# Kernel tuning notes

Measured on AMD Instinct MI355X. Metric: run time of the kernel, lower is better.

## Reference

```python
import jax, jax.numpy as jnp
import numpy as np

B, T, C = 2, 1024, 384
H, D = 4, 96            # heads, head_dim
BLK, NG = 16, 24        # HBS block size, num groups (NG*BLK == C)
SQ, PADM = 20, 400      # monarch grid dim, padded monarch dim
E, K, FF = 8, 2, 1536   # experts, top_k, expert hidden
EPS_LN = 1e-5


def _ln(x, g, b):
    m = jnp.mean(x, -1, keepdims=True)
    v = jnp.var(x, -1, keepdims=True)
    return (x - m) * jax.lax.rsqrt(v + EPS_LN) * g + b


def _hbs(x, pre_g, pre_b, blocks, wrow, wcol, alpha, bias):
    """HierarchicalBlockShuffleLayer: block mixing + flip + monarch, fp32."""
    orig = x.shape
    flat = _ln(x, pre_g, pre_b).astype(jnp.float32).reshape(-1, C)
    # block mixing: per-group 16x16 matmuls
    grouped = flat.reshape(-1, NG, BLK)
    y = jnp.einsum('ngb,gbc->ngc', grouped, blocks).reshape(-1, C)
    block_out = y[:, ::-1]  # torch.flip(dims=[-1])
    # monarch: pad to 400, view as 20x20 grid, left/right mix
    grid = jnp.pad(flat, ((0, 0), (0, PADM - C))).reshape(-1, SQ, SQ)
    z = jnp.einsum('nij,jk,lk->nil', grid, wcol, wrow)  # (x @ W_col) @ W_row.T
    mon = z.reshape(-1, PADM)[:, :C]
    out = block_out + alpha * mon + bias
    return out.reshape(orig)


def _rotary(t_len, d):
    inv = 1.0 / (10000.0 ** (jnp.arange(0, d, 2, dtype=jnp.float32) / d))
    fr = jnp.outer(jnp.arange(t_len, dtype=jnp.float32), inv)  # [T, d/2]
    emb = jnp.concatenate([fr, fr], -1)                        # [T, d]
    return jnp.cos(emb), jnp.sin(emb)


def _rotate_half(x):
    x1, x2 = x[..., : x.shape[-1] // 2], x[..., x.shape[-1] // 2:]
    return jnp.concatenate([-x2, x1], -1)


def _attention(xn, qkv_w, qkv_b, proj_pre_g, proj_pre_b, proj_blocks,
               proj_wrow, proj_wcol, proj_alpha, proj_bias,
               attn_norm_g, attn_norm_b, out_norm_g, out_norm_b, focus_gate):
    qkv = xn @ qkv_w + qkv_b  # [B,T,3C]
    q, k, v = jnp.split(qkv, 3, axis=-1)
    q = q.reshape(B, T, H, D).transpose(0, 2, 1, 3)  # bhtd
    k = k.reshape(B, T, H, D).transpose(0, 2, 1, 3)
    v = v.reshape(B, T, H, D).transpose(0, 2, 1, 3)
    cos, sin = _rotary(T, D)
    cos, sin = cos[None, None], sin[None, None]
    q = q * cos + _rotate_half(q) * sin
    k = k * cos + _rotate_half(k) * sin
    scale = 1.0 / jnp.sqrt(jnp.float32(D))
    # ---- linear attention branch (fp32, cumsum recurrence) ----
    Qp = jax.nn.elu(q * scale) + 1.0
    Kp = jax.nn.elu(k * scale) + 1.0
    KV = Kp[..., :, None] * v[..., None, :]          # bhtde
    KVc = jnp.cumsum(KV, axis=2)
    Kc = jnp.cumsum(Kp, axis=2)
    num = jnp.einsum('bhtd,bhtde->bhte', Qp, KVc)
    den = jnp.einsum('bhtd,bhtd->bht', Qp, Kc)[..., None]
    y_lin = num / (den + 1e-4)
    y_lin = _ln(y_lin, attn_norm_g, attn_norm_b)     # LN over head_dim
    # ---- sharp causal SDPA branch ----
    scores = jnp.einsum('bhtd,bhsd->bhts', q, k) * scale
    mask = jnp.tril(jnp.ones((T, T), dtype=bool))
    scores = jnp.where(mask, scores, -jnp.inf)
    y_sharp = jnp.einsum('bhts,bhsd->bhtd', jax.nn.softmax(scores, -1), v)
    # ---- gated combine ----
    a = jax.nn.sigmoid(focus_gate)
    y = a * y_sharp + (1.0 - a) * y_lin
    y = y.transpose(0, 2, 1, 3).reshape(B, T, C)
    y = _ln(y, out_norm_g, out_norm_b)
    return _hbs(y, proj_pre_g, proj_pre_b, proj_blocks, proj_wrow, proj_wcol,
                proj_alpha, proj_bias)


def _moe(xn, gate_w, w1, b1, w2, b2):
    xf = xn.reshape(-1, C)  # [N,C]
    logits = jnp.clip(xf @ gate_w, -20.0, 20.0)
    w, idx = jax.lax.top_k(logits, K)
    w = jax.nn.softmax(w, -1)
    # dense per-token expert weights [N,E] (same math as sparse dispatch, eval mode)
    wfull = jnp.sum(jax.nn.one_hot(idx, E, dtype=xf.dtype) * w[..., None], axis=1)
    h = jax.nn.gelu(jnp.einsum('nc,ech->neh', xf, w1) + b1, approximate=False)
    o = jnp.einsum('neh,ehc->nec', h, w2) + b2
    out = jnp.einsum('nec,ne->nc', o, wfull)
    return out.reshape(B, T, C)


def setup_inputs() -> dict:
    key = jax.random.key(0)
    ks = jax.random.split(key, 10)
    s = 0.02
    return {
        'x': jax.random.normal(ks[0], (B, T, C), jnp.float32),
        'ln1_g': jnp.ones((C,), jnp.float32), 'ln1_b': jnp.zeros((C,), jnp.float32),
        'ln2_g': jnp.ones((C,), jnp.float32), 'ln2_b': jnp.zeros((C,), jnp.float32),
        'qkv_w': jax.random.normal(ks[1], (C, 3 * C), jnp.float32) * s,
        'qkv_b': jnp.zeros((3 * C,), jnp.float32),
        'proj_pre_g': jnp.ones((C,), jnp.float32), 'proj_pre_b': jnp.zeros((C,), jnp.float32),
        'proj_blocks': jax.random.normal(ks[2], (NG, BLK, BLK), jnp.float32) * 0.125,
        'proj_wrow': jax.random.normal(ks[3], (SQ, SQ), jnp.float32) * 0.05,
        'proj_wcol': jax.random.normal(ks[4], (SQ, SQ), jnp.float32) * 0.05,
        'proj_alpha': jnp.zeros((), jnp.float32),
        'proj_bias': jnp.zeros((C,), jnp.float32),
        'attn_norm_g': jnp.ones((D,), jnp.float32), 'attn_norm_b': jnp.zeros((D,), jnp.float32),
        'out_norm_g': jnp.ones((C,), jnp.float32), 'out_norm_b': jnp.zeros((C,), jnp.float32),
        'focus_gate': jnp.zeros((), jnp.float32),
        'gate_w': jax.random.normal(ks[5], (C, E), jnp.float32) * s,
        'moe_w1': jax.random.normal(ks[6], (E, C, FF), jnp.float32) * s,
        'moe_b1': jnp.zeros((E, FF), jnp.float32),
        'moe_w2': jax.random.normal(ks[7], (E, FF, C), jnp.float32) * s,
        'moe_b2': jnp.zeros((E, C), jnp.float32),
    }


def reference(x, ln1_g, ln1_b, ln2_g, ln2_b, qkv_w, qkv_b,
              proj_pre_g, proj_pre_b, proj_blocks, proj_wrow, proj_wcol,
              proj_alpha, proj_bias, attn_norm_g, attn_norm_b,
              out_norm_g, out_norm_b, focus_gate, gate_w,
              moe_w1, moe_b1, moe_w2, moe_b2):
    h = x + _attention(_ln(x, ln1_g, ln1_b), qkv_w, qkv_b, proj_pre_g, proj_pre_b,
                       proj_blocks, proj_wrow, proj_wcol, proj_alpha, proj_bias,
                       attn_norm_g, attn_norm_b, out_norm_g, out_norm_b, focus_gate)
    out = h + _moe(_ln(h, ln2_g, ln2_b), gate_w, moe_w1, moe_b1, moe_w2, moe_b2)
    return out
```

## Files before the change

### kernel.cpp

```cpp
#include <hip/hip_runtime.h>
#include <math.h>

#define BB 2
#define TT 1024
#define CC 384
#define HH 4
#define DD 96
#define EE 8
#define FFD 1536
#define NROW (BB*TT)
#define QKVN (3*CC)
#define NSLOT (NROW*2)

typedef float f32x4 __attribute__((ext_vector_type(4)));
typedef short bf16x8 __attribute__((ext_vector_type(8)));

__device__ __forceinline__ float wredSum64(float v) {
#pragma unroll
  for (int o = 32; o > 0; o >>= 1) v += __shfl_xor(v, o, 64);
  return v;
}
__device__ __forceinline__ float rsum16(float v) {
#pragma unroll
  for (int o = 8; o > 0; o >>= 1) v += __shfl_xor(v, o, 16);
  return v;
}
__device__ __forceinline__ float rmax16(float v) {
#pragma unroll
  for (int o = 8; o > 0; o >>= 1) v = fmaxf(v, __shfl_xor(v, o, 16));
  return v;
}
__device__ __forceinline__ float dot4f(const float4 a, const float4 b) {
  return a.x*b.x + a.y*b.y + a.z*b.z + a.w*b.w;
}
__device__ __forceinline__ float blockRed128(float v, float* red) {
  v = wredSum64(v);
  const int w = threadIdx.x >> 6;
  if ((threadIdx.x & 63) == 0) red[w] = v;
  __syncthreads();
  float r = red[0] + red[1];
  __syncthreads();
  return r;
}
__device__ __forceinline__ float elup1(float x) {
  return x > 0.f ? x + 1.f : expf(x);
}
__device__ __forceinline__ unsigned short f2bf(float f) {
  unsigned int u = __float_as_uint(f);
  u = (u + 0x7FFFu + ((u >> 16) & 1u)) >> 16;
  return (unsigned short)u;
}

__global__ void zero_counts_kernel(int* counts) {
  if (threadIdx.x < EE) counts[threadIdx.x] = 0;
}

__global__ __launch_bounds__(256) void transconv_kernel(
    const float* __restrict__ src, unsigned short* __restrict__ dst,
    int K, int N) {
  src += (size_t)blockIdx.z * K * N;
  dst += (size_t)blockIdx.z * K * N;
  const int k0 = blockIdx.y * 32, n0 = blockIdx.x * 32;
  __shared__ float tile[32][33];
  const int t = threadIdx.x;
  const int ki = t >> 3, nj = (t & 7) * 4;
  const float4 v = *(const float4*)&src[(size_t)(k0 + ki) * N + n0 + nj];
  tile[ki][nj] = v.x; tile[ki][nj + 1] = v.y;
  tile[ki][nj + 2] = v.z; tile[ki][nj + 3] = v.w;
  __syncthreads();
  const int ni = t >> 3, kj = (t & 7) * 4;
  ushort4 o;
  o.x = f2bf(tile[kj][ni]);     o.y = f2bf(tile[kj + 1][ni]);
  o.z = f2bf(tile[kj + 2][ni]); o.w = f2bf(tile[kj + 3][ni]);
  *(ushort4*)&dst[(size_t)(n0 + ni) * K + k0 + kj] = o;
}

__global__ __launch_bounds__(64) void ln_row_kernel(
    const float* __restrict__ xin, const float* __restrict__ g,
    const float* __restrict__ b, float* __restrict__ xout) {
  const int row = blockIdx.x;
  const int lane = threadIdx.x;
  const size_t base = (size_t)row * CC;
  float v[6];
#pragma unroll
  for (int p = 0; p < 6; ++p) v[p] = xin[base + lane + 64 * p];
  float s = v[0] + v[1] + v[2] + v[3] + v[4] + v[5];
  s = wredSum64(s);
  const float mu = s * (1.f / CC);
  float sq = 0.f;
#pragma unroll
  for (int p = 0; p < 6; ++p) { float d = v[p] - mu; sq += d * d; }
  sq = wredSum64(sq);
  const float rinv = rsqrtf(sq * (1.f / CC) + 1e-5f);
#pragma unroll
  for (int p = 0; p < 6; ++p) {
    const int c = lane + 64 * p;
    xout[base + c] = (v[p] - mu) * rinv * g[c] + b[c];
  }
}

__global__ __launch_bounds__(256) void gemm_qkv_kernel(
    const float* __restrict__ A, const float* __restrict__ Bw,
    const float* __restrict__ bias, float* __restrict__ Cout) {
  const int N = QKVN, K = CC;
  const int n0 = blockIdx.x * 64, m0 = blockIdx.y * 64;
  __shared__ float As[16][68];
  __shared__ float Bs[16][64];
  const int tid = threadIdx.x, tx = tid & 15, ty = tid >> 4;
  const int am = tid >> 2, akq = (tid & 3) * 4;
  const int bkk = tid >> 4, bn4 = (tid & 15) * 4;
  float acc[4][4] = {};
  for (int k0 = 0; k0 < K; k0 += 16) {
    const float4 av4 = *(const float4*)&A[(size_t)(m0 + am) * K + k0 + akq];
    As[akq + 0][am] = av4.x; As[akq + 1][am] = av4.y;
    As[akq + 2][am] = av4.z; As[akq + 3][am] = av4.w;
    *(float4*)&Bs[bkk][bn4] =
        *(const float4*)&Bw[(size_t)(k0 + bkk) * N + n0 + bn4];
    __syncthreads();
#pragma unroll
    for (int kk = 0; kk < 16; ++kk) {
      const float4 av = *(const float4*)&As[kk][ty * 4];
      const float4 bv = *(const float4*)&Bs[kk][tx * 4];
      const float aa[4] = {av.x, av.y, av.z, av.w};
      const float bb4[4] = {bv.x, bv.y, bv.z, bv.w};
#pragma unroll
      for (int i = 0; i < 4; ++i)
#pragma unroll
        for (int jj = 0; jj < 4; ++jj) acc[i][jj] += aa[i] * bb4[jj];
    }
    __syncthreads();
  }
#pragma unroll
  for (int i = 0; i < 4; ++i) {
    const int r = m0 + ty * 4 + i;
#pragma unroll
    for (int jj = 0; jj < 4; ++jj) {
      const int c = n0 + tx * 4 + jj;
      Cout[(size_t)r * N + c] = acc[i][jj] + bias[c];
    }
  }
}

__global__ __launch_bounds__(256) void rope_kernel(
    const float* __restrict__ qkv, float* __restrict__ qr, float* __restrict__ kr,
    float* __restrict__ qp, float* __restrict__ kp) {
  const int gid = blockIdx.x * 256 + threadIdx.x;
  const int i = gid % 48;
  const int t = (gid / 48) % TT;
  const int h = (gid / (48 * TT)) % HH;
  const int b = gid / (48 * TT * HH);
  const float inv = 1.0f / powf(10000.0f, (float)i * (1.0f / 48.0f));
  const float ang = (float)t * inv;
  float sn, cs;
  sincosf(ang, &sn, &cs);
  const float* row = qkv + ((size_t)(b * TT + t)) * QKVN + h * DD;
  const float q1 = row[i], q2 = row[i + 48];
  const float k1 = row[CC + i], k2 = row[CC + i + 48];
  const float qo1 = q1 * cs - q2 * sn, qo2 = q2 * cs + q1 * sn;
  const float ko1 = k1 * cs - k2 * sn, ko2 = k2 * cs + k1 * sn;
  const size_t ob = ((size_t)((b * HH + h) * TT + t)) * DD;
  qr[ob + i] = qo1; qr[ob + i + 48] = qo2;
  kr[ob + i] = ko1; kr[ob + i + 48] = ko2;
  const float scale = 0.10206207261596577f;
  qp[ob + i] = elup1(qo1 * scale); qp[ob + i + 48] = elup1(qo2 * scale);
  kp[ob + i] = elup1(ko1 * scale); kp[ob + i + 48] = elup1(ko2 * scale);
}

__global__ __launch_bounds__(128, 3) void attn_kernel(
    const float* __restrict__ qr, const float* __restrict__ kr,
    const float* __restrict__ qp, const float* __restrict__ kp,
    const float* __restrict__ qkv, const float* __restrict__ ang,
    const float* __restrict__ anb, const float* __restrict__ fgp,
    float* __restrict__ y_attn) {
  __shared__ float Qt[16][100];
  __shared__ float Qpt[16][100];
  __shared__ float Kt[32][100];
  __shared__ float Kpt[32][100];
  __shared__ float Vt[32][100];
  __shared__ float Ps[16][34];
  __shared__ float Pl[16][34];
  const int idx = blockIdx.x;
  const int qt = 63 - (idx >> 3);
  const int bh = idx & 7, b = bh >> 2, h = bh & 3;
  const int tid = threadIdx.x;
  const int j = tid & 15;
  const int r = tid >> 4;
  const float a = 1.f / (1.f + expf(-fgp[0]));
  const int t0 = qt << 4;
  const size_t qbase = ((size_t)bh * TT + t0) * DD;
#pragma unroll
  for (int p = 0; p < 3; ++p) {
    const int i4 = tid + 128 * p, s = i4 / 24, d4 = (i4 % 24) * 4;
    *(float4*)&Qt[s][d4]  = *(const float4*)&qr[qbase + i4 * 4];
    *(float4*)&Qpt[s][d4] = *(const float4*)&qp[qbase + i4 * 4];
  }
  float accS[2][6] = {}, accN[2][6] = {};
  float mrow[2] = {-1e30f, -1e30f}, lrow[2] = {0.f, 0.f}, den[2] = {0.f, 0.f};
  const int nc = (qt >> 1) + 1;
  __syncthreads();
  for (int c = 0; c < nc; ++c) {
    const int s0 = c << 5;
    const float* vb = qkv + ((size_t)(b * TT + s0)) * QKVN + 2 * CC + h * DD;
    const size_t kb = ((size_t)bh * TT + s0) * DD;
#pragma unroll
    for (int p = 0; p < 6; ++p) {
      const int i4 = tid + 128 * p, s = i4 / 24, d4 = (i4 % 24) * 4;
      *(float4*)&Kt[s][d4]  = *(const float4*)&kr[kb + i4 * 4];
      *(float4*)&Kpt[s][d4] = *(const float4*)&kp[kb + i4 * 4];
      *(float4*)&Vt[s][d4]  = *(const float4*)&vb[(size_t)s * QKVN + d4];
    }
    __syncthreads();
    float ds00 = 0, ds01 = 0, ds10 = 0, ds11 = 0;
    float dl00 = 0, dl01 = 0, dl10 = 0, dl11 = 0;
#pragma unroll
    for (int dd = 0; dd < 96; dd += 4) {
      const float4 qa = *(const float4*)&Qt[r][dd];
      const float4 qb = *(const float4*)&Qt[r + 8][dd];
      const float4 ka = *(const float4*)&Kt[j][dd];
      const float4 k2 = *(const float4*)&Kt[j + 16][dd];
      ds00 += dot4f(qa, ka); ds01 += dot4f(qa, k2);
      ds10 += dot4f(qb, ka); ds11 += dot4f(qb, k2);
      const float4 pa = *(const float4*)&Qpt[r][dd];
      const float4 pb = *(const float4*)&Qpt[r + 8][dd];
      const float4 fa = *(const float4*)&Kpt[j][dd];
      const float4 f2 = *(const float4*)&Kpt[j + 16][dd];
      dl00 += dot4f(pa, fa); dl01 += dot4f(pa, f2);
      dl10 += dot4f(pb, fa); dl11 += dot4f(pb, f2);
    }
    const float scale = 0.10206207261596577f;
    float sc00 = ds00 * scale, sc01 = ds01 * scale;
    float sc10 = ds10 * scale, sc11 = ds11 * scale;
    if (c == nc - 1) {
      if (s0 + j > t0 + r)          { sc00 = -1e30f; dl00 = 0.f; }
      if (s0 + j + 16 > t0 + r)     { sc01 = -1e30f; dl01 = 0.f; }
      if (s0 + j > t0 + r + 8)      { sc10 = -1e30f; dl10 = 0.f; }
      if (s0 + j + 16 > t0 + r + 8) { sc11 = -1e30f; dl11 = 0.f; }
    }
    {
      const float cm = rmax16(fmaxf(sc00, sc01));
      const float mn = fmaxf(mrow[0], cm);
      const float sf = expf(mrow[0] - mn);
      const float p0 = expf(sc00 - mn), p1 = expf(sc01 - mn);
      lrow[0] = lrow[0] * sf + rsum16(p0 + p1);
      mrow[0] = mn;
      den[0] += rsum16(dl00 + dl01);
#pragma unroll
      for (int u = 0; u < 6; ++u) accS[0][u] *= sf;
      Ps[r][j] = p0; Ps[r][j + 16] = p1;
      Pl[r][j] = dl00; Pl[r][j + 16] = dl01;
    }
    {
      const float cm = rmax16(fmaxf(sc10, sc11));
      const float mn = fmaxf(mrow[1], cm);
      const float sf = expf(mrow[1] - mn);
      const float p0 = expf(sc10 - mn), p1 = expf(sc11 - mn);
      lrow[1] = lrow[1] * sf + rsum16(p0 + p1);
      mrow[1] = mn;
      den[1] += rsum16(dl10 + dl11);
#pragma unroll
      for (int u = 0; u < 6; ++u) accS[1][u] *= sf;
      Ps[r + 8][j] = p0; Ps[r + 8][j + 16] = p1;
      Pl[r + 8][j] = dl10; Pl[r + 8][j + 16] = dl11;
    }
    __syncthreads();
    const int c0 = j * 6;
#pragma unroll
    for (int s = 0; s < 32; s += 2) {
      const float2 pA = *(const float2*)&Ps[r][s];
      const float2 pB = *(const float2*)&Ps[r + 8][s];
      const float2 lA = *(const float2*)&Pl[r][s];
      const float2 lB = *(const float2*)&Pl[r + 8][s];
      const float* v0p = &Vt[s][c0];
      const float* v1p = v0p + 100;
      float va[6], vb2[6];
      *(float2*)&va[0] = *(const float2*)(v0p);
      *(float2*)&va[2] = *(const float2*)(v0p + 2);
      *(float2*)&va[4] = *(const float2*)(v0p + 4);
      *(float2*)&vb2[0] = *(const float2*)(v1p);
      *(float2*)&vb2[2] = *(const float2*)(v1p + 2);
      *(float2*)&vb2[4] = *(const float2*)(v1p + 4);
#pragma unroll
      for (int u = 0; u < 6; ++u) {
        accS[0][u] += pA.x * va[u] + pA.y * vb2[u];
        accS[1][u] += pB.x * va[u] + pB.y * vb2[u];
        accN[0][u] += lA.x * va[u] + lA.y * vb2[u];
        accN[1][u] += lB.x * va[u] + lB.y * vb2[u];
      }
    }
    __syncthreads();
  }
#pragma unroll
  for (int ri = 0; ri < 2; ++ri) {
    const int t = t0 + r + 8 * ri;
    const float invl = 1.0f / lrow[ri];
    const float dinv = 1.0f / (den[ri] + 1e-4f);
    float yl[6];
    float s1 = 0.f;
#pragma unroll
    for (int u = 0; u < 6; ++u) { yl[u] = accN[ri][u] * dinv; s1 += yl[u]; }
    s1 = rsum16(s1);
    const float mu = s1 * (1.f / DD);
    float s2 = 0.f;
#pragma unroll
    for (int u = 0; u < 6; ++u) { const float d = yl[u] - mu; s2 += d * d; }
    s2 = rsum16(s2);
    const float rr = rsqrtf(s2 * (1.f / DD) + 1e-5f);
    const size_t ob = ((size_t)(b * TT + t)) * CC + h * DD + j * 6;
#pragma unroll
    for (int u = 0; u < 6; ++u) {
      const float ylin = (yl[u] - mu) * rr * ang[j * 6 + u] + anb[j * 6 + u];
      const float ys = accS[ri][u] * invl;
      y_attn[ob + u] = a * ys + (1.f - a) * ylin;
    }
  }
}

__global__ __launch_bounds__(128) void hbs_kernel(
    const float* __restrict__ y_attn, const float* __restrict__ x,
    const float* __restrict__ outg, const float* __restrict__ outb,
    const float* __restrict__ preg, const float* __restrict__ preb,
    const float* __restrict__ blocks, const float* __restrict__ wrow,
    const float* __restrict__ wcol, const float* __restrict__ alphap,
    const float* __restrict__ biasv, const float* __restrict__ ln2g,
    const float* __restrict__ ln2b, const float* __restrict__ gatew,
    float* __restrict__ hout, unsigned short* __restrict__ xn2,
    int* __restrict__ tok_idx, float* __restrict__ tok_w, int* __restrict__ counts) {
  __shared__ float flatS[CC];
  __shared__ float ybuf[CC];
  __shared__ float xbuf[CC];
  __shared__ float tmp[400];
  __shared__ float red[2];
  __shared__ float logit[EE];
  const int row = blockIdx.x, tid = threadIdx.x;
  const size_t base = (size_t)row * CC;
  float v[3];
#pragma unroll
  for (int p = 0; p < 3; ++p) v[p] = y_attn[base + tid + 128 * p];
  float s = blockRed128(v[0] + v[1] + v[2], red);
  float mu = s * (1.f / CC);
  float sq = 0.f;
#pragma unroll
  for (int p = 0; p < 3; ++p) { const float d = v[p] - mu; sq += d * d; }
  sq = blockRed128(sq, red);
  float rin = rsqrtf(sq * (1.f / CC) + 1e-5f);
  float w[3];
#pragma unroll
  for (int p = 0; p < 3; ++p) {
    const int c = tid + 128 * p;
    w[p] = (v[p] - mu) * rin * outg[c] + outb[c];
  }
  s = blockRed128(w[0] + w[1] + w[2], red);
  mu = s * (1.f / CC);
  sq = 0.f;
#pragma unroll
  for (int p = 0; p < 3; ++p) { const float d = w[p] - mu; sq += d * d; }
  sq = blockRed128(sq, red);
  rin = rsqrtf(sq * (1.f / CC) + 1e-5f);
#pragma unroll
  for (int p = 0; p < 3; ++p) {
    const int c = tid + 128 * p;
    flatS[c] = (w[p] - mu) * rin * preg[c] + preb[c];
  }
  __syncthreads();
#pragma unroll
  for (int p = 0; p < 3; ++p) {
    const int o = tid + 128 * p;
    const int g = o >> 4, cc = o & 15;
    const float* bp = blocks + g * 256 + cc;
    const float* fp = flatS + g * 16;
    float acc = 0.f;
#pragma unroll
    for (int bb = 0; bb < 16; ++bb) acc += fp[bb] * bp[bb * 16];
    ybuf[o] = acc;
  }
#pragma unroll
  for (int p = 0; p < 4; ++p) {
    const int o = tid + 128 * p;
    if (o < 400) {
      const int i = o / 20, k = o - i * 20;
      float acc = 0.f;
#pragma unroll
      for (int jj = 0; jj < 20; ++jj) {
        const int src = i * 20 + jj;
        const float gv = (src < CC) ? flatS[src] : 0.f;
        acc += gv * wcol[jj * 20 + k];
      }
      tmp[o] = acc;
    }
  }
  __syncthreads();
  const float alpha = alphap[0];
  float hr[3];
#pragma unroll
  for (int p = 0; p < 3; ++p) {
    const int o = tid + 128 * p;
    const int i = o / 20, ll = o - i * 20;
    float mon = 0.f;
#pragma unroll
    for (int k = 0; k < 20; ++k) mon += tmp[i * 20 + k] * wrow[ll * 20 + k];
    const float hb = ybuf[383 - o] + alpha * mon + biasv[o];
    const float hv = x[base + o] + hb;
    hout[base + o] = hv;
    hr[p] = hv;
  }
  s = blockRed128(hr[0] + hr[1] + hr[2], red);
  mu = s * (1.f / CC);
  sq = 0.f;
#pragma unroll
  for (int p = 0; p < 3; ++p) { const float d = hr[p] - mu; sq += d * d; }
  sq = blockRed128(sq, red);
  rin = rsqrtf(sq * (1.f / CC) + 1e-5f);
#pragma unroll
  for (int p = 0; p < 3; ++p) {
    const int c = tid + 128 * p;
    const float xv = (hr[p] - mu) * rin * ln2g[c] + ln2b[c];
    xn2[base + c] = f2bf(xv);
    xbuf[c] = xv;
  }
  __syncthreads();
  const int e = tid >> 4, jj = tid & 15;
  float part = 0.f;
  for (int c = jj; c < CC; c += 16) part += xbuf[c] * gatew[c * EE + e];
  part = rsum16(part);
  if (jj == 0) logit[e] = fminf(20.f, fmaxf(-20.f, part));
  __syncthreads();
  if (tid == 0) {
    float lg[EE];
#pragma unroll
    for (int ee = 0; ee < EE; ++ee) lg[ee] = logit[ee];
    int i0 = 0; float v0 = lg[0];
#pragma unroll
    for (int ee = 1; ee < EE; ++ee) if (lg[ee] > v0) { v0 = lg[ee]; i0 = ee; }
    int i1 = -1; float v1 = -1e30f;
#pragma unroll
    for (int ee = 0; ee < EE; ++ee)
      if (ee != i0 && lg[ee] > v1) { v1 = lg[ee]; i1 = ee; }
    const float e1 = expf(v1 - v0);
    const float w0 = 1.f / (1.f + e1), w1 = e1 / (1.f + e1);
    tok_idx[2 * row] = i0; tok_idx[2 * row + 1] = i1;
    tok_w[2 * row] = w0; tok_w[2 * row + 1] = w1;
    atomicAdd(&counts[i0], 1);
    atomicAdd(&counts[i1], 1);
  }
}

__global__ void r_offsets_kernel(const int* __restrict__ counts, int* offsets, int* cursor) {
  if (threadIdx.x == 0) {
    int acc = 0;
    for (int e = 0; e < EE; ++e) { offsets[e] = acc; cursor[e] = acc; acc += counts[e]; }
  }
}
__global__ __launch_bounds__(256) void r_scatter_kernel(
    const int* __restrict__ tok_idx, const float* __restrict__ tok_w,
    int* cursor, int* __restrict__ perm, float* __restrict__ slotw,
    int* __restrict__ dest) {
  const int n = blockIdx.x * 256 + threadIdx.x;
  if (n >= NROW) return;
#pragma unroll
  for (int k = 0; k < 2; ++k) {
    const int e = tok_idx[2 * n + k];
    const int pos = atomicAdd(&cursor[e], 1);
    perm[pos] = n;
    slotw[pos] = tok_w[2 * n + k];
    dest[pos] = 2 * n + k;
  }
}


__global__ __launch_bounds__(256) void gemm_moe1_kernel(
    const unsigned short* __restrict__ xn2b, const unsigned short* __restrict__ w1t,
    const float* __restrict__ b1, const int* __restrict__ perm,
    const int* __restrict__ offsets, const int* __restrict__ counts,
    unsigned short* __restrict__ hbuf) {
  const int e = blockIdx.z;
  const int cnt = counts[e];
  const int m0 = blockIdx.y * 64;
  if (m0 >= cnt) return;
  const int n0 = blockIdx.x * 64;
  const int off = offsets[e];
  __shared__ __align__(16) short As[64][40];
  __shared__ __align__(16) short Bs[64][40];
  const int t = threadIdx.x;
  const int srow = t >> 2, sko = (t & 3) * 8;
  const int w = t >> 6, lane = t & 63, lm = lane & 15, kg8 = (lane >> 4) * 8;
  const int wr = (w >> 1) * 32, wc = (w & 1) * 32;
  const int sm = m0 + srow;
  const int grow = perm[off + (sm < cnt ? sm : cnt - 1)];
  const unsigned short* aro = xn2b + (size_t)grow * CC;
  const unsigned short* bro = w1t + ((size_t)e * FFD + n0 + srow) * CC;
  f32x4 acc[2][2] = {};
  for (int k0 = 0; k0 < CC; k0 += 32) {
    *(float4*)&As[srow][sko] = *(const float4*)(aro + k0 + sko);
    *(float4*)&Bs[srow][sko] = *(const float4*)(bro + k0 + sko);
    __syncthreads();
    const bf16x8 a0 = *(const bf16x8*)&As[wr + lm][kg8];
    const bf16x8 a1 = *(const bf16x8*)&As[wr + lm + 16][kg8];
    const bf16x8 b0 = *(const bf16x8*)&Bs[wc + lm][kg8];
    const bf16x8 b1v = *(const bf16x8*)&Bs[wc + lm + 16][kg8];
    acc[0][0] = __builtin_amdgcn_mfma_f32_16x16x32_bf16(a0, b0, acc[0][0], 0, 0, 0);
    acc[0][1] = __builtin_amdgcn_mfma_f32_16x16x32_bf16(a0, b1v, acc[0][1], 0, 0, 0);
    acc[1][0] = __builtin_amdgcn_mfma_f32_16x16x32_bf16(a1, b0, acc[1][0], 0, 0, 0);
    acc[1][1] = __builtin_amdgcn_mfma_f32_16x16x32_bf16(a1, b1v, acc[1][1], 0, 0, 0);
    __syncthreads();
  }
#pragma unroll
  for (int mi = 0; mi < 2; ++mi)
#pragma unroll
    for (int r = 0; r < 4; ++r) {
      const int m = m0 + wr + mi * 16 + (lane >> 4) * 4 + r;
      if (m < cnt) {
#pragma unroll
        for (int ni = 0; ni < 2; ++ni) {
          const int c = n0 + wc + ni * 16 + lm;
          const float tv = acc[mi][ni][r] + b1[e * FFD + c];
          const float gel = 0.5f * tv * (1.0f + erff(tv * 0.70710678118654752f));
          hbuf[(size_t)(off + m) * FFD + c] = f2bf(gel);
        }
      }
    }
}

__global__ __launch_bounds__(256) void gemm_moe2_kernel(
    const unsigned short* __restrict__ hbuf, const unsigned short* __restrict__ w2t,
    const float* __restrict__ b2, const int* __restrict__ offsets,
    const int* __restrict__ counts, const int* __restrict__ dest,
    const float* __restrict__ slotw, float* __restrict__ so) {
  const int e = blockIdx.z;
  const int cnt = counts[e];
  const int m0 = blockIdx.y * 64;
  if (m0 >= cnt) return;
  const int n0 = blockIdx.x * 64;
  const int off = offsets[e];
  __shared__ __align__(16) short As[64][40];
  __shared__ __align__(16) short Bs[64][40];
  const int t = threadIdx.x;
  const int srow = t >> 2, sko = (t & 3) * 8;
  const int w = t >> 6, lane = t & 63, lm = lane & 15, kg8 = (lane >> 4) * 8;
  const int wr = (w >> 1) * 32, wc = (w & 1) * 32;
  const int sm = m0 + srow;
  const unsigned short* aro = hbuf + (size_t)(off + (sm < cnt ? sm : cnt - 1)) * FFD;
  const unsigned short* bro = w2t + ((size_t)e * CC + n0 + srow) * FFD;
  f32x4 acc[2][2] = {};
  for (int k0 = 0; k0 < FFD; k0 += 32) {
    *(float4*)&As[srow][sko] = *(const float4*)(aro + k0 + sko);
    *(float4*)&Bs[srow][sko] = *(const float4*)(bro + k0 + sko);
    __syncthreads();
    const bf16x8 a0 = *(const bf16x8*)&As[wr + lm][kg8];
    const bf16x8 a1 = *(const bf16x8*)&As[wr + lm + 16][kg8];
    const bf16x8 b0 = *(const bf16x8*)&Bs[wc + lm][kg8];
    const bf16x8 b1v = *(const bf16x8*)&Bs[wc + lm + 16][kg8];
    acc[0][0] = __builtin_amdgcn_mfma_f32_16x16x32_bf16(a0, b0, acc[0][0], 0, 0, 0);
    acc[0][1] = __builtin_amdgcn_mfma_f32_16x16x32_bf16(a0, b1v, acc[0][1], 0, 0, 0);
    acc[1][0] = __builtin_amdgcn_mfma_f32_16x16x32_bf16(a1, b0, acc[1][0], 0, 0, 0);
    acc[1][1] = __builtin_amdgcn_mfma_f32_16x16x32_bf16(a1, b1v, acc[1][1], 0, 0, 0);
    __syncthreads();
  }
#pragma unroll
  for (int mi = 0; mi < 2; ++mi)
#pragma unroll
    for (int r = 0; r < 4; ++r) {
      const int m = m0 + wr + mi * 16 + (lane >> 4) * 4 + r;
      if (m < cnt) {
        const int sIdx = off + m;
        const int dd = dest[sIdx];
        const float wv = slotw[sIdx];
#pragma unroll
        for (int ni = 0; ni < 2; ++ni) {
          const int c = n0 + wc + ni * 16 + lm;
          so[(size_t)dd * CC + c] = wv * (acc[mi][ni][r] + b2[e * CC + c]);
        }
      }
    }
}

__global__ __launch_bounds__(256) void final_kernel(
    const float* __restrict__ h, const float* __restrict__ so,
    float* __restrict__ out) {
  const int i = blockIdx.x * 256 + threadIdx.x;
  const int n = i / 96, c = i - n * 96;
  const float4* h4 = (const float4*)h;
  const float4* s4 = (const float4*)so;
  float4* o4 = (float4*)out;
  const float4 a = h4[i];
  const float4 b0 = s4[(size_t)n * 192 + c];
  const float4 b1 = s4[(size_t)n * 192 + 96 + c];
  o4[i] = make_float4(a.x + b0.x + b1.x, a.y + b0.y + b1.y,
                      a.z + b0.z + b1.z, a.w + b0.w + b1.w);
}

extern "C" void kernel_launch(void* const* d_in, const int* in_sizes, int n_in,
                              void* d_out, int out_size, void* d_ws, size_t ws_size,
                              hipStream_t stream) {
  const float* x          = (const float*)d_in[0];
  const float* ln1_g      = (const float*)d_in[1];
  const float* ln1_b      = (const float*)d_in[2];
  const float* ln2_g      = (const float*)d_in[3];
  const float* ln2_b      = (const float*)d_in[4];
  const float* qkv_w      = (const float*)d_in[5];
  const float* qkv_b      = (const float*)d_in[6];
  const float* pre_g      = (const float*)d_in[7];
  const float* pre_b      = (const float*)d_in[8];
  const float* blocks     = (const float*)d_in[9];
  const float* wrow       = (const float*)d_in[10];
  const float* wcol       = (const float*)d_in[11];
  const float* alpha      = (const float*)d_in[12];
  const float* biasv      = (const float*)d_in[13];
  const float* ang        = (const float*)d_in[14];
  const float* anb        = (const float*)d_in[15];
  const float* outg       = (const float*)d_in[16];
  const float* outb       = (const float*)d_in[17];
  const float* fg         = (const float*)d_in[18];
  const float* gatew      = (const float*)d_in[19];
  const float* w1         = (const float*)d_in[20];
  const float* b1         = (const float*)d_in[21];
  const float* w2         = (const float*)d_in[22];
  const float* b2         = (const float*)d_in[23];
  float* out = (float*)d_out;

  char* ws = (char*)d_ws;
  constexpr size_t SZ_ROWC  = (size_t)NROW * CC * 4;
  constexpr size_t SZ_QKV   = (size_t)NROW * QKVN * 4;
  constexpr size_t SZ_HEAD  = (size_t)BB * HH * TT * DD * 4;
  constexpr size_t SZ_HMID  = (size_t)NSLOT * FFD * 4;
  constexpr size_t OFF_A    = 0;
  constexpr size_t OFF_B    = OFF_A + SZ_ROWC;
  constexpr size_t OFF_QR   = OFF_B + SZ_QKV;
  constexpr size_t OFF_KR   = OFF_QR + SZ_HEAD;
  constexpr size_t OFF_QP   = OFF_KR + SZ_HEAD;
  constexpr size_t OFF_KP   = OFF_QP + SZ_HEAD;
  constexpr size_t OFF_HB   = OFF_B + SZ_HMID;
  constexpr size_t OFF_XN2  = OFF_HB + SZ_ROWC;
  constexpr size_t OFF_SO   = OFF_XN2 + SZ_ROWC;
  constexpr size_t OFF_TI   = OFF_SO + (size_t)NSLOT * CC * 4;
  constexpr size_t OFF_TW   = OFF_TI + NSLOT * 4;
  constexpr size_t OFF_PERM = OFF_TW + NSLOT * 4;
  constexpr size_t OFF_SW   = OFF_PERM + NSLOT * 4;
  constexpr size_t OFF_DEST = OFF_SW + NSLOT * 4;
  constexpr size_t OFF_CNT  = OFF_DEST + NSLOT * 4;
  constexpr size_t OFF_OFFS = OFF_CNT + 256;
  constexpr size_t OFF_CUR  = OFF_OFFS + 256;
  constexpr size_t OFF_W1T  = OFF_CUR + 256;
  constexpr size_t OFF_W2T  = OFF_W1T + (size_t)EE * FFD * CC * 2;

  float* xn    = (float*)(ws + OFF_A);
  float* yat   = (float*)(ws + OFF_A);
  float* qkv   = (float*)(ws + OFF_B);
  float* qr    = (float*)(ws + OFF_QR);
  float* kr    = (float*)(ws + OFF_KR);
  float* qp    = (float*)(ws + OFF_QP);
  float* kp    = (float*)(ws + OFF_KP);
  unsigned short* hmid = (unsigned short*)(ws + OFF_B);
  float* hbufr = (float*)(ws + OFF_HB);
  unsigned short* xn2b = (unsigned short*)(ws + OFF_XN2);
  float* so    = (float*)(ws + OFF_SO);
  int*   tok_idx = (int*)(ws + OFF_TI);
  float* tok_w   = (float*)(ws + OFF_TW);
  int*   perm    = (int*)(ws + OFF_PERM);
  float* slotw   = (float*)(ws + OFF_SW);
  int*   dest    = (int*)(ws + OFF_DEST);
  int*   counts  = (int*)(ws + OFF_CNT);
  int*   offsets = (int*)(ws + OFF_OFFS);
  int*   cursor  = (int*)(ws + OFF_CUR);
  unsigned short* w1T  = (unsigned short*)(ws + OFF_W1T);
  unsigned short* w2T  = (unsigned short*)(ws + OFF_W2T);

  zero_counts_kernel<<<1, 64, 0, stream>>>(counts);
  transconv_kernel<<<dim3(FFD / 32, CC / 32, EE), 256, 0, stream>>>(w1, w1T, CC, FFD);
  transconv_kernel<<<dim3(CC / 32, FFD / 32, EE), 256, 0, stream>>>(w2, w2T, FFD, CC);
  ln_row_kernel<<<NROW, 64, 0, stream>>>(x, ln1_g, ln1_b, xn);
  gemm_qkv_kernel<<<dim3(QKVN / 64, NROW / 64), 256, 0, stream>>>(xn, qkv_w, qkv_b, qkv);
  rope_kernel<<<(BB * HH * TT * 48) / 256, 256, 0, stream>>>(qkv, qr, kr, qp, kp);
  attn_kernel<<<dim3(512), 128, 0, stream>>>(qr, kr, qp, kp, qkv, ang, anb, fg, yat);
  hbs_kernel<<<NROW, 128, 0, stream>>>(yat, x, outg, outb, pre_g, pre_b, blocks,
                                       wrow, wcol, alpha, biasv, ln2_g, ln2_b,
                                       gatew, hbufr, xn2b, tok_idx, tok_w, counts);
  r_offsets_kernel<<<1, 64, 0, stream>>>(counts, offsets, cursor);
  r_scatter_kernel<<<NROW / 256, 256, 0, stream>>>(tok_idx, tok_w, cursor, perm, slotw, dest);
  gemm_moe1_kernel<<<dim3(FFD / 64, NROW / 64, EE), 256, 0, stream>>>(
      xn2b, w1T, b1, perm, offsets, counts, hmid);
  gemm_moe2_kernel<<<dim3(CC / 64, NROW / 64, EE), 256, 0, stream>>>(
      hmid, w2T, b2, offsets, counts, dest, slotw, so);
  final_kernel<<<(NROW * CC / 4) / 256, 256, 0, stream>>>(hbufr, so, out);
}
```

Before: 510.5 us.

## Pair short and long causal query tiles per block sharing K/V loads

The attention kernel now runs 256 threads per block, and each block processes two query tiles (qt = 63-pk and qt = pk) for the same batch-head. The two 128-thread groups share one K/Kp/V shared-memory chunk per iteration. Pairing a long tile with a short one balances causal work across blocks and halves grid size. K/V loads are shared within a block, so the short tile's chunks are loaded only once. The short-tile group sits idle at barriers once its chunks are done, and the grid drops to 256 blocks, which may leave CUs underused.

```diff
diff --git a/kernel.cpp b/kernel.cpp
--- a/kernel.cpp
+++ b/kernel.cpp
@@ -166,125 +166,133 @@
   kp[ob + i] = elup1(ko1 * scale); kp[ob + i + 48] = elup1(ko2 * scale);
 }
 
-__global__ __launch_bounds__(128, 3) void attn_kernel(
+__global__ __launch_bounds__(256, 2) void attn_kernel(
     const float* __restrict__ qr, const float* __restrict__ kr,
     const float* __restrict__ qp, const float* __restrict__ kp,
     const float* __restrict__ qkv, const float* __restrict__ ang,
     const float* __restrict__ anb, const float* __restrict__ fgp,
     float* __restrict__ y_attn) {
-  __shared__ float Qt[16][100];
-  __shared__ float Qpt[16][100];
+  __shared__ float Qt[2][16][100];
+  __shared__ float Qpt[2][16][100];
   __shared__ float Kt[32][100];
   __shared__ float Kpt[32][100];
   __shared__ float Vt[32][100];
-  __shared__ float Ps[16][34];
-  __shared__ float Pl[16][34];
-  const int idx = blockIdx.x;
-  const int qt = 63 - (idx >> 3);
-  const int bh = idx & 7, b = bh >> 2, h = bh & 3;
+  __shared__ float Ps[2][16][34];
+  __shared__ float Pl[2][16][34];
+  const int pk = blockIdx.x;
+  const int bh = blockIdx.y, b = bh >> 2, h = bh & 3;
   const int tid = threadIdx.x;
-  const int j = tid & 15;
-  const int r = tid >> 4;
+  const int grp = tid >> 7;
+  const int lt = tid & 127;
+  const int j = lt & 15;
+  const int r = lt >> 4;
+  const int qt = grp ? pk : (63 - pk);
+  const int nc_g = (qt >> 1) + 1;
+  const int ncA = ((63 - pk) >> 1) + 1;
+  const int t0 = qt << 4;
   const float a = 1.f / (1.f + expf(-fgp[0]));
-  const int t0 = qt << 4;
   const size_t qbase = ((size_t)bh * TT + t0) * DD;
 #pragma unroll
   for (int p = 0; p < 3; ++p) {
-    const int i4 = tid + 128 * p, s = i4 / 24, d4 = (i4 % 24) * 4;
-    *(float4*)&Qt[s][d4]  = *(const float4*)&qr[qbase + i4 * 4];
-    *(float4*)&Qpt[s][d4] = *(const float4*)&qp[qbase + i4 * 4];
+    const int i4 = lt + 128 * p, s = i4 / 24, d4 = (i4 % 24) * 4;
+    *(float4*)&Qt[grp][s][d4]  = *(const float4*)&qr[qbase + i4 * 4];
+    *(float4*)&Qpt[grp][s][d4] = *(const float4*)&qp[qbase + i4 * 4];
   }
   float accS[2][6] = {}, accN[2][6] = {};
   float mrow[2] = {-1e30f, -1e30f}, lrow[2] = {0.f, 0.f}, den[2] = {0.f, 0.f};
-  const int nc = (qt >> 1) + 1;
-  __syncthreads();
-  for (int c = 0; c < nc; ++c) {
+  __syncthreads();
+  for (int c = 0; c < ncA; ++c) {
     const int s0 = c << 5;
     const float* vb = qkv + ((size_t)(b * TT + s0)) * QKVN + 2 * CC + h * DD;
     const size_t kb = ((size_t)bh * TT + s0) * DD;
 #pragma unroll
-    for (int p = 0; p < 6; ++p) {
-      const int i4 = tid + 128 * p, s = i4 / 24, d4 = (i4 % 24) * 4;
+    for (int p = 0; p < 3; ++p) {
+      const int i4 = tid + 256 * p, s = i4 / 24, d4 = (i4 % 24) * 4;
       *(float4*)&Kt[s][d4]  = *(const float4*)&kr[kb + i4 * 4];
       *(float4*)&Kpt[s][d4] = *(const float4*)&kp[kb + i4 * 4];
       *(float4*)&Vt[s][d4]  = *(const float4*)&vb[(size_t)s * QKVN + d4];
     }
     __syncthreads();
-    float ds00 = 0, ds01 = 0, ds10 = 0, ds11 = 0;
-    float dl00 = 0, dl01 = 0, dl10 = 0, dl11 = 0;
-#pragma unroll
-    for (int dd = 0; dd < 96; dd += 4) {
-      const float4 qa = *(const float4*)&Qt[r][dd];
-      const float4 qb = *(const float4*)&Qt[r + 8][dd];
-      const float4 ka = *(const float4*)&Kt[j][dd];
-      const float4 k2 = *(const float4*)&Kt[j + 16][dd];
-      ds00 += dot4f(qa, ka); ds01 += dot4f(qa, k2);
-      ds10 += dot4f(qb, ka); ds11 += dot4f(qb, k2);
-      const float4 pa = *(const float4*)&Qpt[r][dd];
-      const float4 pb = *(const float4*)&Qpt[r + 8][dd];
-      const float4 fa = *(const float4*)&Kpt[j][dd];
-      const float4 f2 = *(const float4*)&Kpt[j + 16][dd];
-      dl00 += dot4f(pa, fa); dl01 += dot4f(pa, f2);
-      dl10 += dot4f(pb, fa); dl11 += dot4f(pb, f2);
-    }
-    const float scale = 0.10206207261596577f;
-    float sc00 = ds00 * scale, sc01 = ds01 * scale;
-    float sc10 = ds10 * scale, sc11 = ds11 * scale;
-    if (c == nc - 1) {
-      if (s0 + j > t0 + r)          { sc00 = -1e30f; dl00 = 0.f; }
-      if (s0 + j + 16 > t0 + r)     { sc01 = -1e30f; dl01 = 0.f; }
-      if (s0 + j > t0 + r + 8)      { sc10 = -1e30f; dl10 = 0.f; }
-      if (s0 + j + 16 > t0 + r + 8) { sc11 = -1e30f; dl11 = 0.f; }
-    }
-    {
-      const float cm = rmax16(fmaxf(sc00, sc01));
-      const float mn = fmaxf(mrow[0], cm);
-      const float sf = expf(mrow[0] - mn);
-      const float p0 = expf(sc00 - mn), p1 = expf(sc01 - mn);
-      lrow[0] = lrow[0] * sf + rsum16(p0 + p1);
-      mrow[0] = mn;
-      den[0] += rsum16(dl00 + dl01);
-#pragma unroll
-      for (int u = 0; u < 6; ++u) accS[0][u] *= sf;
-      Ps[r][j] = p0; Ps[r][j + 16] = p1;
-      Pl[r][j] = dl00; Pl[r][j + 16] = dl01;
-    }
-    {
-      const float cm = rmax16(fmaxf(sc10, sc11));
-      const float mn = fmaxf(mrow[1], cm);
-      const float sf = expf(mrow[1] - mn);
-      const float p0 = expf(sc10 - mn), p1 = expf(sc11 - mn);
-      lrow[1] = lrow[1] * sf + rsum16(p0 + p1);
-      mrow[1] = mn;
-      den[1] += rsum16(dl10 + dl11);
-#pragma unroll
-      for (int u = 0; u < 6; ++u) accS[1][u] *= sf;
-      Ps[r + 8][j] = p0; Ps[r + 8][j + 16] = p1;
-      Pl[r + 8][j] = dl10; Pl[r + 8][j + 16] = dl11;
-    }
-    __syncthreads();
-    const int c0 = j * 6;
-#pragma unroll
-    for (int s = 0; s < 32; s += 2) {
-      const float2 pA = *(const float2*)&Ps[r][s];
-      const float2 pB = *(const float2*)&Ps[r + 8][s];
-      const float2 lA = *(const float2*)&Pl[r][s];
-      const float2 lB = *(const float2*)&Pl[r + 8][s];
-      const float* v0p = &Vt[s][c0];
-      const float* v1p = v0p + 100;
-      float va[6], vb2[6];
-      *(float2*)&va[0] = *(const float2*)(v0p);
-      *(float2*)&va[2] = *(const float2*)(v0p + 2);
-      *(float2*)&va[4] = *(const float2*)(v0p + 4);
-      *(float2*)&vb2[0] = *(const float2*)(v1p);
-      *(float2*)&vb2[2] = *(const float2*)(v1p + 2);
-      *(float2*)&vb2[4] = *(const float2*)(v1p + 4);
-#pragma unroll
-      for (int u = 0; u < 6; ++u) {
-        accS[0][u] += pA.x * va[u] + pA.y * vb2[u];
-        accS[1][u] += pB.x * va[u] + pB.y * vb2[u];
-        accN[0][u] += lA.x * va[u] + lA.y * vb2[u];
-        accN[1][u] += lB.x * va[u] + lB.y * vb2[u];
+    const bool act = (c < nc_g);
+    if (act) {
+      float ds00 = 0, ds01 = 0, ds10 = 0, ds11 = 0;
+      float dl00 = 0, dl01 = 0, dl10 = 0, dl11 = 0;
+#pragma unroll
+      for (int dd = 0; dd < 96; dd += 4) {
+        const float4 qa = *(const float4*)&Qt[grp][r][dd];
+        const float4 qb = *(const float4*)&Qt[grp][r + 8][dd];
+        const float4 ka = *(const float4*)&Kt[j][dd];
+        const float4 k2 = *(const float4*)&Kt[j + 16][dd];
+        ds00 += dot4f(qa, ka); ds01 += dot4f(qa, k2);
+        ds10 += dot4f(qb, ka); ds11 += dot4f(qb, k2);
+        const float4 pa = *(const float4*)&Qpt[grp][r][dd];
+        const float4 pb = *(const float4*)&Qpt[grp][r + 8][dd];
+        const float4 fa = *(const float4*)&Kpt[j][dd];
+        const float4 f2 = *(const float4*)&Kpt[j + 16][dd];
+        dl00 += dot4f(pa, fa); dl01 += dot4f(pa, f2);
+        dl10 += dot4f(pb, fa); dl11 += dot4f(pb, f2);
+      }
+      const float scale = 0.10206207261596577f;
+      float sc00 = ds00 * scale, sc01 = ds01 * scale;
+      float sc10 = ds10 * scale, sc11 = ds11 * scale;
+      if (c == nc_g - 1) {
+        if (s0 + j > t0 + r)          { sc00 = -1e30f; dl00 = 0.f; }
+        if (s0 + j + 16 > t0 + r)     { sc01 = -1e30f; dl01 = 0.f; }
+        if (s0 + j > t0 + r + 8)      { sc10 = -1e30f; dl10 = 0.f; }
+        if (s0 + j + 16 > t0 + r + 8) { sc11 = -1e30f; dl11 = 0.f; }
+      }
+      {
+        const float cm = rmax16(fmaxf(sc00, sc01));
+        const float mn = fmaxf(mrow[0], cm);
+        const float sf = expf(mrow[0] - mn);
+        const float p0 = expf(sc00 - mn), p1 = expf(sc01 - mn);
+        lrow[0] = lrow[0] * sf + rsum16(p0 + p1);
+        mrow[0] = mn;
+        den[0] += rsum16(dl00 + dl01);
+#pragma unroll
+        for (int u = 0; u < 6; ++u) accS[0][u] *= sf;
+        Ps[grp][r][j] = p0; Ps[grp][r][j + 16] = p1;
+        Pl[grp][r][j] = dl00; Pl[grp][r][j + 16] = dl01;
+      }
+      {
+        const float cm = rmax16(fmaxf(sc10, sc11));
+        const float mn = fmaxf(mrow[1], cm);
+        const float sf = expf(mrow[1] - mn);
+        const float p0 = expf(sc10 - mn), p1 = expf(sc11 - mn);
+        lrow[1] = lrow[1] * sf + rsum16(p0 + p1);
+        mrow[1] = mn;
+        den[1] += rsum16(dl10 + dl11);
+#pragma unroll
+        for (int u = 0; u < 6; ++u) accS[1][u] *= sf;
+        Ps[grp][r + 8][j] = p0; Ps[grp][r + 8][j + 16] = p1;
+        Pl[grp][r + 8][j] = dl10; Pl[grp][r + 8][j + 16] = dl11;
+      }
+    }
+    __syncthreads();
+    if (act) {
+      const int c0 = j * 6;
+#pragma unroll
+      for (int s = 0; s < 32; s += 2) {
+        const float2 pA = *(const float2*)&Ps[grp][r][s];
+        const float2 pB = *(const float2*)&Ps[grp][r + 8][s];
+        const float2 lA = *(const float2*)&Pl[grp][r][s];
+        const float2 lB = *(const float2*)&Pl[grp][r + 8][s];
+        const float* v0p = &Vt[s][c0];
+        const float* v1p = v0p + 100;
+        float va[6], vb2[6];
+        *(float2*)&va[0] = *(const float2*)(v0p);
+        *(float2*)&va[2] = *(const float2*)(v0p + 2);
+        *(float2*)&va[4] = *(const float2*)(v0p + 4);
+        *(float2*)&vb2[0] = *(const float2*)(v1p);
+        *(float2*)&vb2[2] = *(const float2*)(v1p + 2);
+        *(float2*)&vb2[4] = *(const float2*)(v1p + 4);
+#pragma unroll
+        for (int u = 0; u < 6; ++u) {
+          accS[0][u] += pA.x * va[u] + pA.y * vb2[u];
+          accS[1][u] += pB.x * va[u] + pB.y * vb2[u];
+          accN[0][u] += lA.x * va[u] + lA.y * vb2[u];
+          accN[1][u] += lB.x * va[u] + lB.y * vb2[u];
+        }
       }
     }
     __syncthreads();
@@ -670,7 +678,7 @@
   ln_row_kernel<<<NROW, 64, 0, stream>>>(x, ln1_g, ln1_b, xn);
   gemm_qkv_kernel<<<dim3(QKVN / 64, NROW / 64), 256, 0, stream>>>(xn, qkv_w, qkv_b, qkv);
   rope_kernel<<<(BB * HH * TT * 48) / 256, 256, 0, stream>>>(qkv, qr, kr, qp, kp);
-  attn_kernel<<<dim3(512), 128, 0, stream>>>(qr, kr, qp, kp, qkv, ang, anb, fg, yat);
+  attn_kernel<<<dim3(32, BB * HH), 256, 0, stream>>>(qr, kr, qp, kp, qkv, ang, anb, fg, yat);
   hbs_kernel<<<NROW, 128, 0, stream>>>(yat, x, outg, outb, pre_g, pre_b, blocks,
                                        wrow, wcol, alpha, biasv, ln2_g, ln2_b,
                                        gatew, hbufr, xn2b, tok_idx, tok_w, counts);
```

Result: slower. 562.0 us (+10.1%).
